# Kernel tuning notes

Hardware: AMD Instinct MI355X
Metric: run time of the kernel (lower is better)

## Reference

```python
import jax, jax.numpy as jnp
import numpy as np

EMB_DIM = 128
WEIGHT_COL = 24

def setup_inputs() -> dict:
    key = jax.random.key(0)
    ks = jax.random.split(key, 9)
    B, S = 8, 4096
    s_in = 1.0 / np.sqrt(EMB_DIM)
    s_out = 1.0 / np.sqrt(WEIGHT_COL)
    return {
        "x": jax.random.normal(ks[0], (B, S, EMB_DIM), dtype=jnp.float32),
        "wQ": jax.random.uniform(ks[1], (EMB_DIM, WEIGHT_COL), jnp.float32, -s_in, s_in),
        "bQ": jax.random.uniform(ks[2], (WEIGHT_COL,), jnp.float32, -s_in, s_in),
        "wK": jax.random.uniform(ks[3], (EMB_DIM, WEIGHT_COL), jnp.float32, -s_in, s_in),
        "bK": jax.random.uniform(ks[4], (WEIGHT_COL,), jnp.float32, -s_in, s_in),
        "wV": jax.random.uniform(ks[5], (EMB_DIM, WEIGHT_COL), jnp.float32, -s_in, s_in),
        "bV": jax.random.uniform(ks[6], (WEIGHT_COL,), jnp.float32, -s_in, s_in),
        "wO": jax.random.uniform(ks[7], (WEIGHT_COL, EMB_DIM), jnp.float32, -s_out, s_out),
        "bO": jax.random.uniform(ks[8], (EMB_DIM,), jnp.float32, -s_out, s_out),
    }

def reference(x, wQ, bQ, wK, bK, wV, bV, wO, bO):
    # projections: [B,S,E] -> [B,S,D]
    Q = x @ wQ + bQ
    K = x @ wK + bK
    V = x @ wV + bV
    # NOTE: source scales by sqrt(emb_dim), not sqrt(weight_col)
    scale = 1.0 / np.sqrt(EMB_DIM).astype(np.float32)
    scores = jnp.einsum('bqd,bkd->bqk', Q, K) * scale  # [B,S,S]
    A = jax.nn.softmax(scores, axis=-1)
    H = jnp.einsum('bqk,bkd->bqd', A, V)               # [B,S,D]
    return H @ wO + bO                                  # [B,S,E]
```

## Files before the change

### kernel.cpp

```cpp
#include <hip/hip_runtime.h>
#include <hip/hip_fp16.h>


#define B_ 8
#define S_ 4096
#define E_ 128
#define D_ 24
#define N_ (B_ * S_)
#define SCALE 0.08838834764831845f
#define LOG2E 1.4426950408889634f

#define NSP 8
#define KCHUNK (S_ / NSP)
#define TK 128
#define NT (KCHUNK / TK)

#define KS_STRIDE 40
#define VS_STRIDE 136
#define HS_STRIDE 40
#define XS_STRIDE 136
#define OS_STRIDE 84

typedef __attribute__((ext_vector_type(8))) short bfrag;
typedef __attribute__((ext_vector_type(4))) float ffrag;

__device__ inline unsigned short f2bf(float f) {
    unsigned int x = __builtin_bit_cast(unsigned int, f);
    return (unsigned short)((x + 0x7fffu + ((x >> 16) & 1u)) >> 16);
}
__device__ inline unsigned int pack2h(float a, float b) {
    unsigned int ua = __builtin_bit_cast(unsigned int, a) + 0x8000u;
    unsigned int ub = __builtin_bit_cast(unsigned int, b) + 0x8000u;
    return __builtin_amdgcn_perm(ub, ua, 0x07060302);
}
__device__ inline unsigned int packh16(float a, float b) {
    return __builtin_bit_cast(unsigned int, __builtin_amdgcn_cvt_pkrtz(a, b));
}

__global__ __launch_bounds__(256) void prep_kernel(
    const float* __restrict__ wQ, const float* __restrict__ bQ,
    const float* __restrict__ wK, const float* __restrict__ bK,
    const float* __restrict__ wV, const float* __restrict__ bV,
    const float* __restrict__ wO,
    unsigned short* __restrict__ Wf, unsigned short* __restrict__ wOf,
    float* __restrict__ bqkv)
{
    const int gtid   = blockIdx.x * 256 + threadIdx.x;
    const int stride = gridDim.x * 256;
    const float qs = SCALE * LOG2E;
    for (int idx = gtid; idx < 4 * 5 * 512; idx += stride) {
        const int j    = idx & 7;
        const int lane = (idx >> 3) & 63;
        const int nt   = (idx >> 9) % 5;
        const int kt   = idx / 2560;
        const int n = nt * 16 + (lane & 15);
        const int k = kt * 32 + ((lane >> 4) << 3) + j;
        float v = 0.0f;
        if (n < 24)      v = wQ[k * 24 + n] * qs;
        else if (n < 48) v = wK[k * 24 + (n - 24)];
        else if (n < 72) v = wV[k * 24 + (n - 48)];
        Wf[idx] = f2bf(v);
    }
    for (int idx = gtid; idx < 8 * 512; idx += stride) {
        const int j    = idx & 7;
        const int lane = (idx >> 3) & 63;
        const int nt   = idx >> 9;
        const int k = ((lane >> 4) << 3) + j;
        const int e = nt * 16 + (lane & 15);
        wOf[idx] = (k < 24) ? f2bf(wO[k * 128 + e]) : (unsigned short)0;
    }
    if (gtid < 80) {
        float v = 0.0f;
        if (gtid < 24)      v = bQ[gtid] * qs;
        else if (gtid < 48) v = bK[gtid - 24];
        else if (gtid < 72) v = bV[gtid - 48];
        bqkv[gtid] = v;
    }
}

__global__ __launch_bounds__(256) void proj_kernel(
    const float* __restrict__ x, const unsigned short* __restrict__ Wf,
    const float* __restrict__ bqkv,
    unsigned short* __restrict__ Qbf, unsigned short* __restrict__ Kbf,
    unsigned short* __restrict__ Vt)
{
    __shared__ float smem[64 * OS_STRIDE];
    unsigned short* xs = (unsigned short*)smem;
    float* os = smem;

    const int tid  = threadIdx.x;
    const int lane = tid & 63;
    const int w    = tid >> 6;
    const int col  = lane & 15;
    const int quad = lane >> 4;
    const int rb   = blockIdx.x * 64;

    #pragma unroll
    for (int i = 0; i < 8; ++i) {
        const int idx = i * 256 + tid;
        const int row = idx >> 5, c4 = idx & 31;
        const float4 xv = *(const float4*)(x + (size_t)(rb + row) * 128 + c4 * 4);
        uint2 h;
        h.x = pack2h(xv.x, xv.y);
        h.y = pack2h(xv.z, xv.w);
        *(uint2*)(&xs[row * XS_STRIDE + c4 * 4]) = h;
    }

    bfrag Wfr[20];
    #pragma unroll
    for (int f = 0; f < 20; ++f)
        Wfr[f] = *(const bfrag*)(Wf + (f * 64 + lane) * 8);

    __syncthreads();

    ffrag acc[5];
    #pragma unroll
    for (int nt = 0; nt < 5; ++nt) acc[nt] = (ffrag){0.f, 0.f, 0.f, 0.f};

    #pragma unroll
    for (int kt = 0; kt < 4; ++kt) {
        const bfrag Af = *(const bfrag*)(&xs[(w * 16 + col) * XS_STRIDE + kt * 32 + quad * 8]);
        #pragma unroll
        for (int nt = 0; nt < 5; ++nt)
            acc[nt] = __builtin_amdgcn_mfma_f32_16x16x32_bf16(Af, Wfr[kt * 5 + nt], acc[nt], 0, 0, 0);
    }

    __syncthreads();

    #pragma unroll
    for (int nt = 0; nt < 5; ++nt) {
        const float bb = bqkv[nt * 16 + col];
        #pragma unroll
        for (int r = 0; r < 4; ++r)
            os[(w * 16 + quad * 4 + r) * OS_STRIDE + nt * 16 + col] = acc[nt][r] + bb;
    }
    __syncthreads();

    {
        const int half  = tid & 1;
        const int row   = (tid >> 1) & 63;
        const int isK   = tid >> 7;
        const int cbase = isK * 24;
        unsigned int pk[8];
        #pragma unroll
        for (int g = 0; g < 8; ++g) {
            const int c0 = half * 16 + g * 2;
            const float f0 = (c0     < 24) ? os[row * OS_STRIDE + cbase + c0]     : 0.0f;
            const float f1 = (c0 + 1 < 24) ? os[row * OS_STRIDE + cbase + c0 + 1] : 0.0f;
            pk[g] = pack2h(f0, f1);
        }
        unsigned short* dst = (isK ? Kbf : Qbf) + (size_t)(rb + row) * 32 + half * 16;
        *(uint4*)(dst)     = make_uint4(pk[0], pk[1], pk[2], pk[3]);
        *(uint4*)(dst + 8) = make_uint4(pk[4], pk[5], pk[6], pk[7]);
    }

    if (tid < 192) {
        const int d  = tid % 24;
        const int ch = tid / 24;
        unsigned int p[4];
        #pragma unroll
        for (int g = 0; g < 4; ++g) {
            const float f0 = os[(ch * 8 + g * 2 + 0) * OS_STRIDE + 48 + d];
            const float f1 = os[(ch * 8 + g * 2 + 1) * OS_STRIDE + 48 + d];
            p[g] = pack2h(f0, f1);
        }
        const int b = rb >> 12, s0 = rb & 4095;
        uint4* dst = (uint4*)(Vt + (((size_t)(b * 32 + d)) << 12) + s0 + ch * 8);
        *dst = make_uint4(p[0], p[1], p[2], p[3]);
    } else if (tid < 200) {
        const int ch = tid - 192;
        const int b = rb >> 12, s0 = rb & 4095;
        uint4* dst = (uint4*)(Vt + (((size_t)(b * 32 + 24)) << 12) + s0 + ch * 8);
        *dst = make_uint4(0x3F803F80u, 0x3F803F80u, 0x3F803F80u, 0x3F803F80u);
    }
}

__global__ __launch_bounds__(512, 6) void attn_kernel(
    const unsigned short* __restrict__ Qbf, const unsigned short* __restrict__ Kbf,
    const unsigned short* __restrict__ Vt,
    __half* __restrict__ Opart, float* __restrict__ lpart)
{
    __shared__ unsigned short Ks[2 * TK * KS_STRIDE];
    __shared__ unsigned short Vs[2 * 25 * VS_STRIDE];

    const int tid   = threadIdx.x;
    const int lane  = tid & 63;
    const int w     = tid >> 6;
    const int col   = lane & 15;
    const int quad  = lane >> 4;
    const int blk   = blockIdx.x;
    const int split = blockIdx.y;
    const int b     = blk >> 4;
    const int qbase = blk * 256 + w * 32;

    const bfrag Qf0 = *(const bfrag*)(Qbf + (size_t)(qbase + col) * 32 + quad * 8);
    const bfrag Qf1 = *(const bfrag*)(Qbf + (size_t)(qbase + 16 + col) * 32 + quad * 8);

    const unsigned short* Kbase = Kbf + ((size_t)b * 4096 + split * KCHUNK) * 32;
    const unsigned short* Vbase = Vt + (size_t)(b * 32) * 4096 + split * KCHUNK;

    const int skey = tid >> 2, sch = tid & 3;
    const int srow = (skey & ~31) + (((skey >> 2) & 1) << 4)
                   + (((skey & 31) >> 3) << 2) + (skey & 3);
    const int sd = tid >> 4, svch = tid & 15;

    const int r1 = (16 + col <= 24) ? (16 + col) : 24;

    ffrag O00 = {0.f,0.f,0.f,0.f};
    ffrag O01 = {0.f,0.f,0.f,0.f};
    ffrag O10 = {0.f,0.f,0.f,0.f};
    ffrag O11 = {0.f,0.f,0.f,0.f};

    auto compute_tile = [&](const unsigned short* ksb, const unsigned short* vsb) {
        #pragma unroll
        for (int c2 = 0; c2 < 4; ++c2) {
            const bfrag Kfe = *(const bfrag*)(&ksb[(c2 * 32 + col) * KS_STRIDE + quad * 8]);
            const bfrag Kfo = *(const bfrag*)(&ksb[(c2 * 32 + 16 + col) * KS_STRIDE + quad * 8]);
            const bfrag Va0 = *(const bfrag*)(&vsb[col * VS_STRIDE + c2 * 32 + quad * 8]);
            const bfrag Va1 = *(const bfrag*)(&vsb[r1 * VS_STRIDE + c2 * 32 + quad * 8]);

            {
                ffrag Se = {0.f,0.f,0.f,0.f}, So = {0.f,0.f,0.f,0.f};
                Se = __builtin_amdgcn_mfma_f32_16x16x32_bf16(Kfe, Qf0, Se, 0, 0, 0);
                So = __builtin_amdgcn_mfma_f32_16x16x32_bf16(Kfo, Qf0, So, 0, 0, 0);
                union { bfrag f; unsigned int u[4]; } P;
                P.u[0] = pack2h(__builtin_amdgcn_exp2f(Se[0]), __builtin_amdgcn_exp2f(Se[1]));
                P.u[1] = pack2h(__builtin_amdgcn_exp2f(Se[2]), __builtin_amdgcn_exp2f(Se[3]));
                P.u[2] = pack2h(__builtin_amdgcn_exp2f(So[0]), __builtin_amdgcn_exp2f(So[1]));
                P.u[3] = pack2h(__builtin_amdgcn_exp2f(So[2]), __builtin_amdgcn_exp2f(So[3]));
                O00 = __builtin_amdgcn_mfma_f32_16x16x32_bf16(Va0, P.f, O00, 0, 0, 0);
                O01 = __builtin_amdgcn_mfma_f32_16x16x32_bf16(Va1, P.f, O01, 0, 0, 0);
            }
            {
                ffrag Se = {0.f,0.f,0.f,0.f}, So = {0.f,0.f,0.f,0.f};
                Se = __builtin_amdgcn_mfma_f32_16x16x32_bf16(Kfe, Qf1, Se, 0, 0, 0);
                So = __builtin_amdgcn_mfma_f32_16x16x32_bf16(Kfo, Qf1, So, 0, 0, 0);
                union { bfrag f; unsigned int u[4]; } P;
                P.u[0] = pack2h(__builtin_amdgcn_exp2f(Se[0]), __builtin_amdgcn_exp2f(Se[1]));
                P.u[1] = pack2h(__builtin_amdgcn_exp2f(Se[2]), __builtin_amdgcn_exp2f(Se[3]));
                P.u[2] = pack2h(__builtin_amdgcn_exp2f(So[0]), __builtin_amdgcn_exp2f(So[1]));
                P.u[3] = pack2h(__builtin_amdgcn_exp2f(So[2]), __builtin_amdgcn_exp2f(So[3]));
                O10 = __builtin_amdgcn_mfma_f32_16x16x32_bf16(Va0, P.f, O10, 0, 0, 0);
                O11 = __builtin_amdgcn_mfma_f32_16x16x32_bf16(Va1, P.f, O11, 0, 0, 0);
            }
        }
    };

    {
        const uint4 k4 = *(const uint4*)(Kbase + (size_t)skey * 32 + sch * 8);
        *(uint4*)(&Ks[srow * KS_STRIDE + sch * 8]) = k4;
        if (tid < 400) {
            const uint4 v4 = *(const uint4*)(Vbase + (size_t)sd * 4096 + svch * 8);
            *(uint4*)(&Vs[sd * VS_STRIDE + svch * 8]) = v4;
        }
    }
    __syncthreads();

    int cur = 0;
    for (int t = 0; t < NT - 1; ++t) {
        const int kb = (t + 1) * TK;
        const uint4 k4 = *(const uint4*)(Kbase + (size_t)(kb + skey) * 32 + sch * 8);
        uint4 v4;
        if (tid < 400)
            v4 = *(const uint4*)(Vbase + (size_t)sd * 4096 + kb + svch * 8);
        __builtin_amdgcn_sched_barrier(0);

        compute_tile(Ks + cur * (TK * KS_STRIDE), Vs + cur * (25 * VS_STRIDE));

        const int nxt = cur ^ 1;
        *(uint4*)(&Ks[nxt * (TK * KS_STRIDE) + srow * KS_STRIDE + sch * 8]) = k4;
        if (tid < 400)
            *(uint4*)(&Vs[nxt * (25 * VS_STRIDE) + sd * VS_STRIDE + svch * 8]) = v4;
        __syncthreads();
        cur = nxt;
    }
    compute_tile(Ks + cur * (TK * KS_STRIDE), Vs + cur * (25 * VS_STRIDE));

    {
        const size_t base0 = ((size_t)split * N_ + qbase + col) * 32;
        uint2 s0;
        s0.x = packh16(O00[0], O00[1]);
        s0.y = packh16(O00[2], O00[3]);
        *(uint2*)(Opart + base0 + quad * 4) = s0;
        if (quad < 2) {
            uint2 s1;
            s1.x = packh16(O01[0], O01[1]);
            s1.y = packh16(O01[2], O01[3]);
            *(uint2*)(Opart + base0 + 16 + quad * 4) = s1;
        }
        if (quad == 2)
            lpart[(size_t)split * N_ + qbase + col] = O01[0];

        const size_t base1 = base0 + 16 * 32;
        uint2 t0;
        t0.x = packh16(O10[0], O10[1]);
        t0.y = packh16(O10[2], O10[3]);
        *(uint2*)(Opart + base1 + quad * 4) = t0;
        if (quad < 2) {
            uint2 t1;
            t1.x = packh16(O11[0], O11[1]);
            t1.y = packh16(O11[2], O11[3]);
            *(uint2*)(Opart + base1 + 16 + quad * 4) = t1;
        }
        if (quad == 2)
            lpart[(size_t)split * N_ + qbase + 16 + col] = O11[0];
    }
}

__global__ __launch_bounds__(256) void combine_kernel(
    const __half* __restrict__ Opart, const float* __restrict__ lpart,
    const unsigned short* __restrict__ wOf, const float* __restrict__ bO,
    float* __restrict__ out)
{
    __shared__ unsigned short Hs[64 * HS_STRIDE];

    const int tid = threadIdx.x;
    const int qb  = blockIdx.x * 64;
    {
        const int ql = tid >> 2;
        const int c8 = (tid & 3) * 8;
        const int q  = qb + ql;
        float a[8] = {0.f, 0.f, 0.f, 0.f, 0.f, 0.f, 0.f, 0.f};
        if (c8 < 24) {
            #pragma unroll
            for (int s = 0; s < NSP; ++s) {
                union { uint4 u; __half2 h[4]; } U;
                U.u = *(const uint4*)(Opart + ((size_t)s * N_ + q) * 32 + c8);
                #pragma unroll
                for (int j = 0; j < 4; ++j) {
                    const float2 f = __half22float2(U.h[j]);
                    a[2 * j]     += f.x;
                    a[2 * j + 1] += f.y;
                }
            }
        }
        float ls = 0.f;
        #pragma unroll
        for (int s = 0; s < NSP; ++s) ls += lpart[(size_t)s * N_ + q];
        const float inv = 1.0f / ls;
        uint4 pk;
        pk.x = pack2h(a[0] * inv, a[1] * inv);
        pk.y = pack2h(a[2] * inv, a[3] * inv);
        pk.z = pack2h(a[4] * inv, a[5] * inv);
        pk.w = pack2h(a[6] * inv, a[7] * inv);
        *(uint4*)(&Hs[ql * HS_STRIDE + c8]) = pk;
    }
    __syncthreads();

    const int lane = tid & 63;
    const int w    = tid >> 6;
    const int col  = lane & 15;
    const int quad = lane >> 4;
    const bfrag Hf = *(const bfrag*)(&Hs[(w * 16 + col) * HS_STRIDE + quad * 8]);
    #pragma unroll
    for (int nt = 0; nt < 8; ++nt) {
        const bfrag Wo = *(const bfrag*)(wOf + (nt * 64 + lane) * 8);
        ffrag C = {0.f, 0.f, 0.f, 0.f};
        C = __builtin_amdgcn_mfma_f32_16x16x32_bf16(Hf, Wo, C, 0, 0, 0);
        const float bo = bO[nt * 16 + col];
        #pragma unroll
        for (int r = 0; r < 4; ++r)
            out[(size_t)(qb + w * 16 + quad * 4 + r) * 128 + nt * 16 + col] = C[r] + bo;
    }
}

extern "C" void kernel_launch(void* const* d_in, const int* in_sizes, int n_in,
                              void* d_out, int out_size, void* d_ws, size_t ws_size,
                              hipStream_t stream) {
    const float* x  = (const float*)d_in[0];
    const float* wQ = (const float*)d_in[1];
    const float* bQ = (const float*)d_in[2];
    const float* wK = (const float*)d_in[3];
    const float* bK = (const float*)d_in[4];
    const float* wV = (const float*)d_in[5];
    const float* bV = (const float*)d_in[6];
    const float* wO = (const float*)d_in[7];
    const float* bO = (const float*)d_in[8];
    float* out = (float*)d_out;

    unsigned short* ws16 = (unsigned short*)d_ws;
    unsigned short* Qbf = ws16;
    unsigned short* Kbf = Qbf + (size_t)N_ * 32;
    unsigned short* Vt  = Kbf + (size_t)N_ * 32;
    unsigned short* Wf  = Vt + (size_t)B_ * 32 * S_;
    unsigned short* wOf = Wf + 4 * 5 * 512;
    float* bqkv = (float*)(wOf + 8 * 512);
    __half* Opart = (__half*)(bqkv + 80);
    float* lpart = (float*)(Opart + (size_t)NSP * N_ * 32);

    prep_kernel<<<8, 256, 0, stream>>>(wQ, bQ, wK, bK, wV, bV, wO, Wf, wOf, bqkv);
    proj_kernel<<<N_ / 64, 256, 0, stream>>>(x, Wf, bqkv, Qbf, Kbf, Vt);
    attn_kernel<<<dim3(N_ / 256, NSP), 512, 0, stream>>>(Qbf, Kbf, Vt, Opart, lpart);
    combine_kernel<<<N_ / 64, 256, 0, stream>>>(Opart, lpart, wOf, bO, out);
}
```

Baseline: 121.8 us.

## Fold weight prep into projection kernel, halve key splits, prioritize MFMA waves

```diff
diff --git a/kernel.cpp b/kernel.cpp
--- a/kernel.cpp
+++ b/kernel.cpp
@@ -10,7 +10,7 @@
 #define SCALE 0.08838834764831845f
 #define LOG2E 1.4426950408889634f
 
-#define NSP 8
+#define NSP 4
 #define KCHUNK (S_ / NSP)
 #define TK 128
 #define NT (KCHUNK / TK)
@@ -37,56 +37,20 @@
     return __builtin_bit_cast(unsigned int, __builtin_amdgcn_cvt_pkrtz(a, b));
 }
 
-__global__ __launch_bounds__(256) void prep_kernel(
+__global__ __launch_bounds__(256) void proj_kernel(
+    const float* __restrict__ x,
     const float* __restrict__ wQ, const float* __restrict__ bQ,
     const float* __restrict__ wK, const float* __restrict__ bK,
     const float* __restrict__ wV, const float* __restrict__ bV,
     const float* __restrict__ wO,
-    unsigned short* __restrict__ Wf, unsigned short* __restrict__ wOf,
-    float* __restrict__ bqkv)
+    unsigned short* __restrict__ Qbf, unsigned short* __restrict__ Kbf,
+    unsigned short* __restrict__ Vt, unsigned short* __restrict__ wOf)
 {
-    const int gtid   = blockIdx.x * 256 + threadIdx.x;
-    const int stride = gridDim.x * 256;
-    const float qs = SCALE * LOG2E;
-    for (int idx = gtid; idx < 4 * 5 * 512; idx += stride) {
-        const int j    = idx & 7;
-        const int lane = (idx >> 3) & 63;
-        const int nt   = (idx >> 9) % 5;
-        const int kt   = idx / 2560;
-        const int n = nt * 16 + (lane & 15);
-        const int k = kt * 32 + ((lane >> 4) << 3) + j;
-        float v = 0.0f;
-        if (n < 24)      v = wQ[k * 24 + n] * qs;
-        else if (n < 48) v = wK[k * 24 + (n - 24)];
-        else if (n < 72) v = wV[k * 24 + (n - 48)];
-        Wf[idx] = f2bf(v);
-    }
-    for (int idx = gtid; idx < 8 * 512; idx += stride) {
-        const int j    = idx & 7;
-        const int lane = (idx >> 3) & 63;
-        const int nt   = idx >> 9;
-        const int k = ((lane >> 4) << 3) + j;
-        const int e = nt * 16 + (lane & 15);
-        wOf[idx] = (k < 24) ? f2bf(wO[k * 128 + e]) : (unsigned short)0;
-    }
-    if (gtid < 80) {
-        float v = 0.0f;
-        if (gtid < 24)      v = bQ[gtid] * qs;
-        else if (gtid < 48) v = bK[gtid - 24];
-        else if (gtid < 72) v = bV[gtid - 48];
-        bqkv[gtid] = v;
-    }
-}
-
-__global__ __launch_bounds__(256) void proj_kernel(
-    const float* __restrict__ x, const unsigned short* __restrict__ Wf,
-    const float* __restrict__ bqkv,
-    unsigned short* __restrict__ Qbf, unsigned short* __restrict__ Kbf,
-    unsigned short* __restrict__ Vt)
-{
-    __shared__ float smem[64 * OS_STRIDE];
-    unsigned short* xs = (unsigned short*)smem;
-    float* os = smem;
+    __shared__ float smem[9552];
+    unsigned short* xs  = (unsigned short*)smem;
+    unsigned short* Ws  = (unsigned short*)smem + 8704;
+    float*          bks = smem + 9472;
+    float*          os  = smem;
 
     const int tid  = threadIdx.x;
     const int lane = tid & 63;
@@ -94,6 +58,7 @@
     const int col  = lane & 15;
     const int quad = lane >> 4;
     const int rb   = blockIdx.x * 64;
+    const float qs = SCALE * LOG2E;
 
     #pragma unroll
     for (int i = 0; i < 8; ++i) {
@@ -106,12 +71,43 @@
         *(uint2*)(&xs[row * XS_STRIDE + c4 * 4]) = h;
     }
 
+    for (int idx = tid; idx < 10240; idx += 256) {
+        const int j    = idx & 7;
+        const int ln   = (idx >> 3) & 63;
+        const int nt   = (idx >> 9) % 5;
+        const int kt   = idx / 2560;
+        const int n = nt * 16 + (ln & 15);
+        const int k = kt * 32 + ((ln >> 4) << 3) + j;
+        float v = 0.0f;
+        if (n < 24)      v = wQ[k * 24 + n] * qs;
+        else if (n < 48) v = wK[k * 24 + (n - 24)];
+        else if (n < 72) v = wV[k * 24 + (n - 48)];
+        Ws[idx] = f2bf(v);
+    }
+    if (tid < 80) {
+        float v = 0.0f;
+        if (tid < 24)      v = bQ[tid] * qs;
+        else if (tid < 48) v = bK[tid - 24];
+        else if (tid < 72) v = bV[tid - 48];
+        bks[tid] = v;
+    }
+    if (blockIdx.x == 0) {
+        for (int idx = tid; idx < 4096; idx += 256) {
+            const int j  = idx & 7;
+            const int ln = (idx >> 3) & 63;
+            const int nt = idx >> 9;
+            const int k = ((ln >> 4) << 3) + j;
+            const int e = nt * 16 + (ln & 15);
+            wOf[idx] = (k < 24) ? f2bf(wO[k * 128 + e]) : (unsigned short)0;
+        }
+    }
+
+    __syncthreads();
+
     bfrag Wfr[20];
     #pragma unroll
     for (int f = 0; f < 20; ++f)
-        Wfr[f] = *(const bfrag*)(Wf + (f * 64 + lane) * 8);
-
-    __syncthreads();
+        Wfr[f] = *(const bfrag*)(Ws + (f * 64 + lane) * 8);
 
     ffrag acc[5];
     #pragma unroll
@@ -129,7 +125,7 @@
 
     #pragma unroll
     for (int nt = 0; nt < 5; ++nt) {
-        const float bb = bqkv[nt * 16 + col];
+        const float bb = bks[nt * 16 + col];
         #pragma unroll
         for (int r = 0; r < 4; ++r)
             os[(w * 16 + quad * 4 + r) * OS_STRIDE + nt * 16 + col] = acc[nt][r] + bb;
@@ -175,7 +171,7 @@
     }
 }
 
-__global__ __launch_bounds__(512, 6) void attn_kernel(
+__global__ __launch_bounds__(512, 4) void attn_kernel(
     const unsigned short* __restrict__ Qbf, const unsigned short* __restrict__ Kbf,
     const unsigned short* __restrict__ Vt,
     __half* __restrict__ Opart, float* __restrict__ lpart)
@@ -212,6 +208,7 @@
     ffrag O11 = {0.f,0.f,0.f,0.f};
 
     auto compute_tile = [&](const unsigned short* ksb, const unsigned short* vsb) {
+        __builtin_amdgcn_s_setprio(1);
         #pragma unroll
         for (int c2 = 0; c2 < 4; ++c2) {
             const bfrag Kfe = *(const bfrag*)(&ksb[(c2 * 32 + col) * KS_STRIDE + quad * 8]);
@@ -244,6 +241,7 @@
                 O11 = __builtin_amdgcn_mfma_f32_16x16x32_bf16(Va1, P.f, O11, 0, 0, 0);
             }
         }
+        __builtin_amdgcn_s_setprio(0);
     };
 
     {
@@ -382,14 +380,12 @@
     unsigned short* Qbf = ws16;
     unsigned short* Kbf = Qbf + (size_t)N_ * 32;
     unsigned short* Vt  = Kbf + (size_t)N_ * 32;
-    unsigned short* Wf  = Vt + (size_t)B_ * 32 * S_;
-    unsigned short* wOf = Wf + 4 * 5 * 512;
-    float* bqkv = (float*)(wOf + 8 * 512);
-    __half* Opart = (__half*)(bqkv + 80);
+    unsigned short* wOf = Vt + (size_t)B_ * 32 * S_;
+    __half* Opart = (__half*)(wOf + 8 * 512);
     float* lpart = (float*)(Opart + (size_t)NSP * N_ * 32);
 
-    prep_kernel<<<8, 256, 0, stream>>>(wQ, bQ, wK, bK, wV, bV, wO, Wf, wOf, bqkv);
-    proj_kernel<<<N_ / 64, 256, 0, stream>>>(x, Wf, bqkv, Qbf, Kbf, Vt);
+    proj_kernel<<<N_ / 64, 256, 0, stream>>>(x, wQ, bQ, wK, bK, wV, bV, wO,
+                                             Qbf, Kbf, Vt, wOf);
     attn_kernel<<<dim3(N_ / 256, NSP), 512, 0, stream>>>(Qbf, Kbf, Vt, Opart, lpart);
     combine_kernel<<<N_ / 64, 256, 0, stream>>>(Opart, lpart, wOf, bO, out);
 }
```

After: 128.4 us. 1.05x slower.
